# Kernel optimization log

Measured on AMD Instinct MI355X. Metric: run time of the kernel, lower is better.

Reference implementation:

```python
import jax, jax.numpy as jnp
import numpy as np

B, HH, WW, C, HEADS = 8, 56, 56, 384, 6
DIM_OUT = 384


def _upsample2x_bilinear(x):
    # x: [..., m, n] -> [..., 2m, 2n]; matches torch F.interpolate bilinear align_corners=False
    m, n = x.shape[-2], x.shape[-1]
    def coords(inn):
        c = (jnp.arange(2 * inn) + 0.5) / 2.0 - 0.5
        c = jnp.clip(c, 0.0, inn - 1)
        i0 = jnp.floor(c).astype(jnp.int32)
        i1 = jnp.minimum(i0 + 1, inn - 1)
        return i0, i1, (c - i0).astype(x.dtype)
    i0, i1, wy = coords(m)
    j0, j1, wx = coords(n)
    rows = x[..., i0, :] * (1 - wy)[:, None] + x[..., i1, :] * wy[:, None]
    return rows[..., :, j0] * (1 - wx) + rows[..., :, j1] * wx


def setup_inputs() -> dict:
    key = jax.random.key(0)
    ks = jax.random.split(key, 12)
    inp = {
        'x': jax.random.normal(ks[0], (B, HH * WW, C), jnp.float32),
        'res_attn': jax.random.normal(ks[1], (B, HEADS, (HH // 4) * (WW // 4), (HH // 2) * (WW // 2)), jnp.float32),
        'conv_q_w': jax.random.normal(ks[2], (C, 1, 3, 3), jnp.float32) * 0.05,
        'ln_g': jnp.ones((C,), jnp.float32),
        'ln_b': jnp.zeros((C,), jnp.float32),
        'wq': jax.random.normal(ks[3], (DIM_OUT, C), jnp.float32) * 0.02,
        'wk': jax.random.normal(ks[4], (DIM_OUT, C), jnp.float32) * 0.02,
        'wv': jax.random.normal(ks[5], (DIM_OUT, C), jnp.float32) * 0.02,
        'w_proj': jax.random.normal(ks[6], (DIM_OUT, DIM_OUT), jnp.float32) * 0.02,
        'b_proj': jnp.zeros((DIM_OUT,), jnp.float32),
        'w_fuse': jax.random.normal(ks[7], (HEADS, 2 * HEADS, 1, 1), jnp.float32) * 0.1,
        'b_fuse': jnp.zeros((HEADS,), jnp.float32),
        'h': HH,
        'w': WW,
    }
    return inp


def reference(x, res_attn, conv_q_w, ln_g, ln_b, wq, wk, wv, w_proj, b_proj, w_fuse, b_fuse, h, w):
    Bz, _, Cc = x.shape
    heads = w_fuse.shape[0]
    xi = x.transpose(0, 2, 1).reshape(Bz, Cc, h, w)  # b c h w
    # conv_proj_q: depthwise conv k3 s2 p1 (no bias), then LayerNorm
    q = jax.lax.conv_general_dilated(
        xi, conv_q_w, (2, 2), ((1, 1), (1, 1)),
        dimension_numbers=('NCHW', 'OIHW', 'NCHW'), feature_group_count=Cc)
    hq, wq2 = q.shape[2], q.shape[3]
    q = q.reshape(Bz, Cc, hq * wq2).transpose(0, 2, 1)  # b t c
    mu = q.mean(-1, keepdims=True)
    var = ((q - mu) ** 2).mean(-1, keepdims=True)
    q = (q - mu) / jnp.sqrt(var + 1e-5) * ln_g + ln_b
    # conv_proj_k/v: avg pool k2 s2 p0
    kv = xi.reshape(Bz, Cc, h // 2, 2, w // 2, 2).mean(axis=(3, 5))
    kv = kv.reshape(Bz, Cc, (h // 2) * (w // 2)).transpose(0, 2, 1)  # b t c
    dim_out = wq.shape[0]
    dh = dim_out // heads
    def split(t):
        return t.reshape(Bz, t.shape[1], heads, dh).transpose(0, 2, 1, 3)
    qh = split(q @ wq.T)
    kh = split(kv @ wk.T)
    vh = split(kv @ wv.T)
    scale = dim_out ** -0.5
    attn_score = jnp.einsum('bhlk,bhtk->bhlt', qh, kh) * scale  # [B,H,L,T]
    sh, sw = h // 4, w // 4
    a = res_attn.shape[-1]
    rx = res_attn[:, :, :sh * sw, :]
    rx = rx.reshape(Bz * heads, sh * sw, a).transpose(0, 2, 1).reshape(Bz * heads, a, sh, sw)
    rx = _upsample2x_bilinear(rx)  # (b h) a 2sh 2sw
    rx = rx.reshape(Bz, heads, a, 4 * sh * sw).transpose(0, 1, 3, 2)  # b h L a
    cat = jnp.concatenate([attn_score, rx], axis=1)  # [B, 2H, L, T]
    attn_score = jnp.einsum('bclt,oc->bolt', cat, w_fuse[:, :, 0, 0]) + b_fuse[None, :, None, None]
    attn = jax.nn.softmax(attn_score, axis=-1)
    out = jnp.einsum('bhlt,bhtv->bhlv', attn, vh)
    out = out.transpose(0, 2, 1, 3).reshape(Bz, -1, dim_out)
    return out @ w_proj.T + b_proj
```

## Files before the change

### kernel.cpp

```cpp
#include <hip/hip_runtime.h>

typedef unsigned int uint;
typedef unsigned short ushort_t;
typedef short bf16x8 __attribute__((ext_vector_type(8)));
typedef float f32x4 __attribute__((ext_vector_type(4)));

__device__ __forceinline__ ushort_t f2bf(float f) {
  uint u = __builtin_bit_cast(uint, f);
  u += 0x7fffu + ((u >> 16) & 1u);
  return (ushort_t)(u >> 16);
}
__device__ __forceinline__ float bf2f(ushort_t s) {
  return __builtin_bit_cast(float, (uint)s << 16);
}
__device__ __forceinline__ float bflo(uint u) { return __builtin_bit_cast(float, u << 16); }
__device__ __forceinline__ float bfhi(uint u) { return __builtin_bit_cast(float, u & 0xffff0000u); }
__device__ __forceinline__ bf16x8 ld_frag(const ushort_t* p) {
  return __builtin_bit_cast(bf16x8, *(const uint4*)p);
}

__global__ __launch_bounds__(384) void k_convln(
    const float* __restrict__ x, const float* __restrict__ wc,
    const float* __restrict__ g, const float* __restrict__ bb,
    ushort_t* __restrict__ qout)
{
  const int b  = blockIdx.x / 784;
  const int t  = blockIdx.x % 784;
  const int oy = t / 28, ox = t % 28;
  const int c  = threadIdx.x;
  const float* xb = x + (size_t)b * 3136 * 384 + c;
  float acc = 0.f;
  #pragma unroll
  for (int ky = 0; ky < 3; ky++) {
    const int iy = 2 * oy - 1 + ky;
    if (iy < 0 || iy >= 56) continue;
    #pragma unroll
    for (int kx = 0; kx < 3; kx++) {
      const int ix = 2 * ox - 1 + kx;
      if (ix < 0 || ix >= 56) continue;
      acc += wc[c * 9 + ky * 3 + kx] * xb[(size_t)(iy * 56 + ix) * 384];
    }
  }
  float s = acc, s2 = acc * acc;
  #pragma unroll
  for (int off = 32; off >= 1; off >>= 1) {
    s  += __shfl_xor(s,  off);
    s2 += __shfl_xor(s2, off);
  }
  __shared__ float ps[6], ps2[6];
  if ((c & 63) == 0) { ps[c >> 6] = s; ps2[c >> 6] = s2; }
  __syncthreads();
  float S = 0.f, S2 = 0.f;
  #pragma unroll
  for (int i = 0; i < 6; i++) { S += ps[i]; S2 += ps2[i]; }
  const float mu  = S * (1.f / 384.f);
  const float var = S2 * (1.f / 384.f) - mu * mu;
  const float inv = rsqrtf(var + 1e-5f);
  qout[((size_t)b * 784 + t) * 384 + c] = f2bf((acc - mu) * inv * g[c] + bb[c]);
}

__global__ __launch_bounds__(256) void k_pool(
    const float* __restrict__ x, ushort_t* __restrict__ kvout)
{
  const int idx = blockIdx.x * 256 + threadIdx.x;
  const int c = idx % 384;
  const int t = (idx / 384) % 784;
  const int b = idx / (384 * 784);
  const int ty = t / 28, tx = t % 28;
  const float* xb = x + (size_t)b * 3136 * 384 + c;
  const int r0 = (2 * ty) * 56 + 2 * tx;
  const float v = xb[(size_t)r0 * 384] + xb[(size_t)(r0 + 1) * 384]
                + xb[(size_t)(r0 + 56) * 384] + xb[(size_t)(r0 + 57) * 384];
  kvout[idx] = f2bf(v * 0.25f);
}

__global__ __launch_bounds__(256) void k_wcvt(
    const float* __restrict__ a, const float* __restrict__ b,
    const float* __restrict__ c, const float* __restrict__ d,
    ushort_t* __restrict__ oa, ushort_t* __restrict__ ob,
    ushort_t* __restrict__ oc, ushort_t* __restrict__ od)
{
  const int i = blockIdx.x * 256 + threadIdx.x;
  if (i < 147456) {
    oa[i] = f2bf(a[i]); ob[i] = f2bf(b[i]);
    oc[i] = f2bf(c[i]); od[i] = f2bf(d[i]);
  }
}

template<int MODE>
__global__ __launch_bounds__(256) void k_gemm(
    const ushort_t* __restrict__ X, const ushort_t* __restrict__ W,
    const float* __restrict__ bias, void* __restrict__ Y)
{
  __shared__ ushort_t As[128][40];
  __shared__ ushort_t Bs[128][40];
  const int tid = threadIdx.x, w = tid >> 6, lane = tid & 63;
  const int quad = lane >> 4, r = lane & 15;
  const int m0 = blockIdx.y * 128, n0 = blockIdx.x * 128;
  const int wm = w >> 1, wn = w & 1;
  const int lr = tid >> 2, lc = (tid & 3) << 3;
  const ushort_t* xp = X + (size_t)(m0 + lr) * 384 + lc;
  const ushort_t* wp = W + (size_t)(n0 + lr) * 384 + lc;
  f32x4 acc[4][4] = {};
  for (int k0 = 0; k0 < 384; k0 += 32) {
    __syncthreads();
    *(uint4*)&As[lr][lc]      = *(const uint4*)(xp + k0);
    *(uint4*)&As[lr + 64][lc] = *(const uint4*)(xp + (size_t)64 * 384 + k0);
    *(uint4*)&Bs[lr][lc]      = *(const uint4*)(wp + k0);
    *(uint4*)&Bs[lr + 64][lc] = *(const uint4*)(wp + (size_t)64 * 384 + k0);
    __syncthreads();
    bf16x8 af[4], bf_[4];
    #pragma unroll
    for (int mt = 0; mt < 4; mt++) af[mt]  = *(const bf16x8*)&As[wm * 64 + mt * 16 + r][quad * 8];
    #pragma unroll
    for (int nt = 0; nt < 4; nt++) bf_[nt] = *(const bf16x8*)&Bs[wn * 64 + nt * 16 + r][quad * 8];
    #pragma unroll
    for (int mt = 0; mt < 4; mt++)
      #pragma unroll
      for (int nt = 0; nt < 4; nt++)
        acc[mt][nt] = __builtin_amdgcn_mfma_f32_16x16x32_bf16(af[mt], bf_[nt], acc[mt][nt], 0, 0, 0);
  }
  #pragma unroll
  for (int mt = 0; mt < 4; mt++) {
    #pragma unroll
    for (int nt = 0; nt < 4; nt++) {
      #pragma unroll
      for (int i = 0; i < 4; i++) {
        const int row = m0 + wm * 64 + mt * 16 + quad * 4 + i;
        const int col = n0 + wn * 64 + nt * 16 + r;
        const float v = acc[mt][nt][i];
        if constexpr (MODE == 2) {
          ((float*)Y)[(size_t)row * 384 + col] = v + bias[col];
        } else if constexpr (MODE == 0) {
          ((ushort_t*)Y)[(size_t)row * 384 + col] = f2bf(v);
        } else {
          const int bb = row / 784, tt = row % 784;
          ((ushort_t*)Y)[((size_t)bb * 384 + col) * 784 + tt] = f2bf(v);
        }
      }
    }
  }
}

__global__ __launch_bounds__(256) void k_resmix(
    const float* __restrict__ ra, const float* __restrict__ w_fuse,
    const float* __restrict__ b_fuse, ushort_t* __restrict__ R)
{
  const int tid = threadIdx.x;
  const int b = blockIdx.x / 784, L = blockIdx.x % 784;
  __shared__ float w2[36], bfu[6];
  if (tid < 36) w2[tid] = w_fuse[(tid / 6) * 12 + 6 + (tid % 6)];
  if (tid < 6)  bfu[tid] = b_fuse[tid];
  __syncthreads();

  const int Yc = L / 28, Xc = L % 28;
  const float cy = fminf(fmaxf((float)Yc * 0.5f - 0.25f, 0.f), 13.f);
  const float cx = fminf(fmaxf((float)Xc * 0.5f - 0.25f, 0.f), 13.f);
  const int y0 = (int)cy, y1 = min(y0 + 1, 13);
  const int x0 = (int)cx, x1 = min(x0 + 1, 13);
  const float fy = cy - (float)y0, fx = cx - (float)x0;
  const float w00 = (1.f - fy) * (1.f - fx), w01 = (1.f - fy) * fx;
  const float w10 = fy * (1.f - fx),         w11 = fy * fx;
  const int p00 = (y0 * 14 + x0) * 784, p01 = (y0 * 14 + x1) * 784;
  const int p10 = (y1 * 14 + x0) * 784, p11 = (y1 * 14 + x1) * 784;

  const float* rab = ra + (size_t)b * 6 * 153664;
  ushort_t* Rrow = R + ((size_t)(b * 784 + L) * 6) * 784;

  for (int t = tid; t < 784; t += 256) {
    float U[6];
    #pragma unroll
    for (int c = 0; c < 6; c++) {
      const float* rc = rab + (size_t)c * 153664;
      U[c] = w00 * rc[p00 + t] + w01 * rc[p01 + t]
           + w10 * rc[p10 + t] + w11 * rc[p11 + t];
    }
    #pragma unroll
    for (int o = 0; o < 6; o++) {
      float v = bfu[o];
      #pragma unroll
      for (int c = 0; c < 6; c++) v += w2[o * 6 + c] * U[c];
      Rrow[(size_t)o * 784 + t] = f2bf(v);
    }
  }
}

__global__ __launch_bounds__(256, 3) void k_fattn(
    const ushort_t* __restrict__ Qb, const ushort_t* __restrict__ Kb,
    const ushort_t* __restrict__ Vt, const ushort_t* __restrict__ R,
    const float* __restrict__ w_fuse,
    float* __restrict__ Op, float* __restrict__ Ms, float* __restrict__ Ss)
{
  __shared__ ushort_t Ssc[6][16][72];
  __shared__ ushort_t Pl[6][16][72];
  __shared__ float m_st[6][16], s_st[6][16], a_st[6][16];
  __shared__ float w1[36];

  const int tid  = threadIdx.x;
  const int w    = tid >> 6, lane = tid & 63;
  const int quad = lane >> 4, r = lane & 15;
  const int b    = blockIdx.x & 7;
  const int m0   = (blockIdx.x >> 3) * 16;
  const int s    = blockIdx.y;
  const int tile0 = (s == 0) ? 0 : (3 * s + 1);
  const int tileN = (s == 0) ? 4 : 3;
  const float scale = 0.05103103630798288f;

  if (tid < 36) w1[tid] = w_fuse[(tid / 6) * 12 + (tid % 6)] * scale;
  if (tid < 96) { (&m_st[0][0])[tid] = -1e30f; (&s_st[0][0])[tid] = 0.f; }

  const ushort_t* qrow = Qb + ((size_t)(b * 784 + m0 + r)) * 384 + quad * 8;
  bf16x8 qf[6][2];
  #pragma unroll
  for (int h = 0; h < 6; h++) {
    qf[h][0] = ld_frag(qrow + h * 64);
    qf[h][1] = ld_frag(qrow + h * 64 + 32);
  }

  const int bl_l = tid >> 4, tq = tid & 15;
  const ushort_t* Rrow = R + ((size_t)(b * 784 + m0 + bl_l) * 6) * 784;

  const size_t kbase  = (size_t)b * 784 * 384;
  const size_t vtbase = (size_t)b * 384 * 784;

  f32x4 oacc[6] = {};

  for (int ii = 0; ii < tileN; ii++) {
    const int t0 = (tile0 + ii) * 64;

    {
      const int tA = min(t0 + w * 16 + r, 783);
      const ushort_t* krow = Kb + kbase + (size_t)tA * 384 + quad * 8;
      #pragma unroll
      for (int h = 0; h < 6; h++) {
        f32x4 sc = {};
        sc = __builtin_amdgcn_mfma_f32_16x16x32_bf16(qf[h][0], ld_frag(krow + h * 64),      sc, 0, 0, 0);
        sc = __builtin_amdgcn_mfma_f32_16x16x32_bf16(qf[h][1], ld_frag(krow + h * 64 + 32), sc, 0, 0, 0);
        #pragma unroll
        for (int i = 0; i < 4; i++)
          Ssc[h][quad * 4 + i][w * 16 + r] = f2bf(sc[i]);
      }
    }
    __syncthreads();

    {
      const int t4 = t0 + tq * 4;
      float F[6][4];
      #pragma unroll
      for (int o = 0; o < 6; o++) {
        const uint2 rv = *(const uint2*)(Rrow + (size_t)o * 784 + t4);
        F[o][0] = bflo(rv.x); F[o][1] = bfhi(rv.x);
        F[o][2] = bflo(rv.y); F[o][3] = bfhi(rv.y);
      }
      #pragma unroll
      for (int c = 0; c < 6; c++) {
        const uint2 sv = *(const uint2*)&Ssc[c][bl_l][tq * 4];
        const float s0 = bflo(sv.x), s1 = bfhi(sv.x);
        const float s2 = bflo(sv.y), s3 = bfhi(sv.y);
        #pragma unroll
        for (int o = 0; o < 6; o++) {
          const float wv = w1[o * 6 + c];
          F[o][0] += wv * s0; F[o][1] += wv * s1;
          F[o][2] += wv * s2; F[o][3] += wv * s3;
        }
      }
      #pragma unroll
      for (int j = 0; j < 4; j++) {
        if (t4 + j >= 784) {
          #pragma unroll
          for (int o = 0; o < 6; o++) F[o][j] = -1e30f;
        }
      }
      #pragma unroll
      for (int o = 0; o < 6; o++) {
        float mx = fmaxf(fmaxf(F[o][0], F[o][1]), fmaxf(F[o][2], F[o][3]));
        #pragma unroll
        for (int off = 8; off >= 1; off >>= 1) mx = fmaxf(mx, __shfl_xor(mx, off));
        const float m_old = m_st[o][bl_l];
        const float nm = fmaxf(m_old, mx);
        const float al = __expf(m_old - nm);
        float p0 = __expf(F[o][0] - nm), p1 = __expf(F[o][1] - nm);
        float p2 = __expf(F[o][2] - nm), p3 = __expf(F[o][3] - nm);
        float sm = p0 + p1 + p2 + p3;
        #pragma unroll
        for (int off = 8; off >= 1; off >>= 1) sm += __shfl_xor(sm, off);
        const uint lo = (uint)f2bf(p0) | ((uint)f2bf(p1) << 16);
        const uint hi = (uint)f2bf(p2) | ((uint)f2bf(p3) << 16);
        *(uint2*)&Pl[o][bl_l][tq * 4] = uint2{lo, hi};
        if (tq == 0) {
          m_st[o][bl_l] = nm;
          s_st[o][bl_l] = s_st[o][bl_l] * al + sm;
          a_st[o][bl_l] = al;
        }
      }
    }
    __syncthreads();

    #pragma unroll
    for (int o = 0; o < 6; o++) {
      const f32x4 al4 = *(const f32x4*)&a_st[o][quad * 4];
      oacc[o] *= al4;
      const bf16x8 pa0 = *(const bf16x8*)&Pl[o][r][quad * 8];
      const bf16x8 pa1 = *(const bf16x8*)&Pl[o][r][quad * 8 + 32];
      const ushort_t* vrow = Vt + vtbase + (size_t)(o * 64 + w * 16 + r) * 784 + t0 + quad * 8;
      oacc[o] = __builtin_amdgcn_mfma_f32_16x16x32_bf16(pa0, ld_frag(vrow),      oacc[o], 0, 0, 0);
      oacc[o] = __builtin_amdgcn_mfma_f32_16x16x32_bf16(pa1, ld_frag(vrow + 32), oacc[o], 0, 0, 0);
    }
    __syncthreads();
  }

  const size_t prow = (size_t)s * 6272 + (size_t)b * 784 + m0;
  #pragma unroll
  for (int o = 0; o < 6; o++) {
    #pragma unroll
    for (int i = 0; i < 4; i++) {
      Op[(prow + quad * 4 + i) * 384 + o * 64 + w * 16 + r] = oacc[o][i];
    }
  }
  if (tid < 96) {
    const int o = tid >> 4, l = tid & 15;
    Ms[(prow + l) * 6 + o] = m_st[o][l];
    Ss[(prow + l) * 6 + o] = s_st[o][l];
  }
}

__global__ __launch_bounds__(256) void k_comb(
    const float* __restrict__ Op, const float* __restrict__ Ms,
    const float* __restrict__ Ss, ushort_t* __restrict__ O)
{
  const int idx = blockIdx.x * 256 + threadIdx.x;
  const int row = idx / 384, col = idx % 384, o = col >> 6;
  float m = -1e30f;
  #pragma unroll
  for (int s = 0; s < 4; s++) m = fmaxf(m, Ms[((size_t)s * 6272 + row) * 6 + o]);
  float S = 0.f, acc = 0.f;
  #pragma unroll
  for (int s = 0; s < 4; s++) {
    const size_t pr = (size_t)s * 6272 + row;
    const float e = __expf(Ms[pr * 6 + o] - m);
    S   += Ss[pr * 6 + o] * e;
    acc += Op[pr * 384 + col] * e;
  }
  O[(size_t)row * 384 + col] = f2bf(acc / S);
}

extern "C" void kernel_launch(void* const* d_in, const int* in_sizes, int n_in,
                              void* d_out, int out_size, void* d_ws, size_t ws_size,
                              hipStream_t stream)
{
  const float* x        = (const float*)d_in[0];
  const float* res_attn = (const float*)d_in[1];
  const float* conv_w   = (const float*)d_in[2];
  const float* ln_g     = (const float*)d_in[3];
  const float* ln_b     = (const float*)d_in[4];
  const float* wq       = (const float*)d_in[5];
  const float* wk       = (const float*)d_in[6];
  const float* wv       = (const float*)d_in[7];
  const float* w_proj   = (const float*)d_in[8];
  const float* b_proj   = (const float*)d_in[9];
  const float* w_fuse   = (const float*)d_in[10];
  const float* b_fuse   = (const float*)d_in[11];
  float* out = (float*)d_out;

  const size_t NE = (size_t)8 * 784 * 384;
  const size_t NW = 147456;
  const size_t NR = (size_t)8 * 784 * 6 * 784;
  ushort_t* q_ln_b = (ushort_t*)d_ws;
  ushort_t* kv_b   = q_ln_b + NE;
  ushort_t* Qb     = kv_b + NE;
  ushort_t* Kb     = Qb + NE;
  ushort_t* Vt     = Kb + NE;
  ushort_t* Opre   = Vt + NE + 64;
  ushort_t* wqb    = Opre + NE;
  ushort_t* wkb    = wqb + NW;
  ushort_t* wvb    = wkb + NW;
  ushort_t* wpb    = wvb + NW;
  ushort_t* R      = wpb + NW;
  float*    Op     = (float*)(R + NR + 512);
  float*    Ms     = Op + 4 * NE;
  float*    Ss     = Ms + 4 * 6272 * 6;

  k_convln<<<dim3(8 * 784), dim3(384), 0, stream>>>(x, conv_w, ln_g, ln_b, q_ln_b);
  k_pool  <<<dim3(9408),    dim3(256), 0, stream>>>(x, kv_b);
  k_wcvt  <<<dim3(576),     dim3(256), 0, stream>>>(wq, wk, wv, w_proj, wqb, wkb, wvb, wpb);
  k_resmix<<<dim3(8 * 784), dim3(256), 0, stream>>>(res_attn, w_fuse, b_fuse, R);

  k_gemm<0><<<dim3(3, 49), dim3(256), 0, stream>>>(q_ln_b, wqb, nullptr, Qb);
  k_gemm<0><<<dim3(3, 49), dim3(256), 0, stream>>>(kv_b,   wkb, nullptr, Kb);
  k_gemm<1><<<dim3(3, 49), dim3(256), 0, stream>>>(kv_b,   wvb, nullptr, Vt);

  k_fattn<<<dim3(392, 4), dim3(256), 0, stream>>>(Qb, Kb, Vt, R, w_fuse, Op, Ms, Ss);
  k_comb <<<dim3(9408),   dim3(256), 0, stream>>>(Op, Ms, Ss, Opre);

  k_gemm<2><<<dim3(3, 49), dim3(256), 0, stream>>>(Opre, wpb, b_proj, out);
}
```

Baseline: 373.4 us.

## Apply residual-attention channel mix before upsampling and upsample inside the attention kernel

The 6x6 head-fusion mix on res_attn now runs at the low 14x14 resolution, writing a bf16 buffer a quarter the size of the old full upsampled R tensor. The attention kernel then does the bilinear 2x upsample on the fly with four gathered loads per element, which removes most of the R write and read traffic. Other changes: conv+LN and 2x2 pooling are merged into one kernel that reuses the conv taps, the V projection is a separate transposed GEMM whose stores are coalesced along tokens, attention partial outputs go through shared memory for float4 stores, and M/S statistics are packed as float2. The tradeoff is more scattered global loads and extra ALU work in the attention inner loop.

```diff
diff --git a/kernel.cpp b/kernel.cpp
--- a/kernel.cpp
+++ b/kernel.cpp
@@ -19,28 +19,32 @@
   return __builtin_bit_cast(bf16x8, *(const uint4*)p);
 }
 
-__global__ __launch_bounds__(384) void k_convln(
+__global__ __launch_bounds__(384) void k_prep(
     const float* __restrict__ x, const float* __restrict__ wc,
     const float* __restrict__ g, const float* __restrict__ bb,
-    ushort_t* __restrict__ qout)
+    ushort_t* __restrict__ qout, ushort_t* __restrict__ kvout)
 {
   const int b  = blockIdx.x / 784;
   const int t  = blockIdx.x % 784;
   const int oy = t / 28, ox = t % 28;
   const int c  = threadIdx.x;
   const float* xb = x + (size_t)b * 3136 * 384 + c;
-  float acc = 0.f;
+  float tap[9];
   #pragma unroll
   for (int ky = 0; ky < 3; ky++) {
     const int iy = 2 * oy - 1 + ky;
-    if (iy < 0 || iy >= 56) continue;
     #pragma unroll
     for (int kx = 0; kx < 3; kx++) {
       const int ix = 2 * ox - 1 + kx;
-      if (ix < 0 || ix >= 56) continue;
-      acc += wc[c * 9 + ky * 3 + kx] * xb[(size_t)(iy * 56 + ix) * 384];
-    }
-  }
+      tap[ky * 3 + kx] = (iy >= 0 && iy < 56 && ix >= 0 && ix < 56)
+                         ? xb[(size_t)(iy * 56 + ix) * 384] : 0.f;
+    }
+  }
+  float acc = 0.f;
+  #pragma unroll
+  for (int k = 0; k < 9; k++) acc += wc[c * 9 + k] * tap[k];
+  const float pool = (tap[4] + tap[5] + tap[7] + tap[8]) * 0.25f;
+
   float s = acc, s2 = acc * acc;
   #pragma unroll
   for (int off = 32; off >= 1; off >>= 1) {
@@ -56,22 +60,9 @@
   const float mu  = S * (1.f / 384.f);
   const float var = S2 * (1.f / 384.f) - mu * mu;
   const float inv = rsqrtf(var + 1e-5f);
-  qout[((size_t)b * 784 + t) * 384 + c] = f2bf((acc - mu) * inv * g[c] + bb[c]);
-}
-
-__global__ __launch_bounds__(256) void k_pool(
-    const float* __restrict__ x, ushort_t* __restrict__ kvout)
-{
-  const int idx = blockIdx.x * 256 + threadIdx.x;
-  const int c = idx % 384;
-  const int t = (idx / 384) % 784;
-  const int b = idx / (384 * 784);
-  const int ty = t / 28, tx = t % 28;
-  const float* xb = x + (size_t)b * 3136 * 384 + c;
-  const int r0 = (2 * ty) * 56 + 2 * tx;
-  const float v = xb[(size_t)r0 * 384] + xb[(size_t)(r0 + 1) * 384]
-                + xb[(size_t)(r0 + 56) * 384] + xb[(size_t)(r0 + 57) * 384];
-  kvout[idx] = f2bf(v * 0.25f);
+  const size_t o = ((size_t)b * 784 + t) * 384 + c;
+  qout[o]  = f2bf((acc - mu) * inv * g[c] + bb[c]);
+  kvout[o] = f2bf(pool);
 }
 
 __global__ __launch_bounds__(256) void k_wcvt(
@@ -84,6 +75,31 @@
   if (i < 147456) {
     oa[i] = f2bf(a[i]); ob[i] = f2bf(b[i]);
     oc[i] = f2bf(c[i]); od[i] = f2bf(d[i]);
+  }
+}
+
+__global__ __launch_bounds__(256) void k_rcmix(
+    const float* __restrict__ ra, const float* __restrict__ w_fuse,
+    ushort_t* __restrict__ RC)
+{
+  const int tid = threadIdx.x;
+  const int b = blockIdx.x / 196, lc = blockIdx.x % 196;
+  __shared__ float w2[36];
+  if (tid < 36) w2[tid] = w_fuse[(tid / 6) * 12 + 6 + (tid % 6)];
+  __syncthreads();
+  const float* rab = ra + ((size_t)b * 6 * 196 + lc) * 784;
+  ushort_t* RCb = RC + ((size_t)b * 6 * 196 + lc) * 784;
+  for (int t = tid; t < 784; t += 256) {
+    float U[6];
+    #pragma unroll
+    for (int c = 0; c < 6; c++) U[c] = rab[(size_t)c * 153664 + t];
+    #pragma unroll
+    for (int o = 0; o < 6; o++) {
+      float v = 0.f;
+      #pragma unroll
+      for (int c = 0; c < 6; c++) v += w2[o * 6 + c] * U[c];
+      RCb[(size_t)o * 153664 + t] = f2bf(v);
+    }
   }
 }
 
@@ -129,72 +145,74 @@
         const int row = m0 + wm * 64 + mt * 16 + quad * 4 + i;
         const int col = n0 + wn * 64 + nt * 16 + r;
         const float v = acc[mt][nt][i];
-        if constexpr (MODE == 2) {
-          ((float*)Y)[(size_t)row * 384 + col] = v + bias[col];
-        } else if constexpr (MODE == 0) {
-          ((ushort_t*)Y)[(size_t)row * 384 + col] = f2bf(v);
-        } else {
-          const int bb = row / 784, tt = row % 784;
-          ((ushort_t*)Y)[((size_t)bb * 384 + col) * 784 + tt] = f2bf(v);
-        }
-      }
-    }
-  }
-}
-
-__global__ __launch_bounds__(256) void k_resmix(
-    const float* __restrict__ ra, const float* __restrict__ w_fuse,
-    const float* __restrict__ b_fuse, ushort_t* __restrict__ R)
-{
-  const int tid = threadIdx.x;
-  const int b = blockIdx.x / 784, L = blockIdx.x % 784;
-  __shared__ float w2[36], bfu[6];
-  if (tid < 36) w2[tid] = w_fuse[(tid / 6) * 12 + 6 + (tid % 6)];
-  if (tid < 6)  bfu[tid] = b_fuse[tid];
-  __syncthreads();
-
-  const int Yc = L / 28, Xc = L % 28;
-  const float cy = fminf(fmaxf((float)Yc * 0.5f - 0.25f, 0.f), 13.f);
-  const float cx = fminf(fmaxf((float)Xc * 0.5f - 0.25f, 0.f), 13.f);
-  const int y0 = (int)cy, y1 = min(y0 + 1, 13);
-  const int x0 = (int)cx, x1 = min(x0 + 1, 13);
-  const float fy = cy - (float)y0, fx = cx - (float)x0;
-  const float w00 = (1.f - fy) * (1.f - fx), w01 = (1.f - fy) * fx;
-  const float w10 = fy * (1.f - fx),         w11 = fy * fx;
-  const int p00 = (y0 * 14 + x0) * 784, p01 = (y0 * 14 + x1) * 784;
-  const int p10 = (y1 * 14 + x0) * 784, p11 = (y1 * 14 + x1) * 784;
-
-  const float* rab = ra + (size_t)b * 6 * 153664;
-  ushort_t* Rrow = R + ((size_t)(b * 784 + L) * 6) * 784;
-
-  for (int t = tid; t < 784; t += 256) {
-    float U[6];
-    #pragma unroll
-    for (int c = 0; c < 6; c++) {
-      const float* rc = rab + (size_t)c * 153664;
-      U[c] = w00 * rc[p00 + t] + w01 * rc[p01 + t]
-           + w10 * rc[p10 + t] + w11 * rc[p11 + t];
-    }
-    #pragma unroll
-    for (int o = 0; o < 6; o++) {
-      float v = bfu[o];
-      #pragma unroll
-      for (int c = 0; c < 6; c++) v += w2[o * 6 + c] * U[c];
-      Rrow[(size_t)o * 784 + t] = f2bf(v);
+        if constexpr (MODE == 2) ((float*)Y)[(size_t)row * 384 + col] = v + bias[col];
+        else                     ((ushort_t*)Y)[(size_t)row * 384 + col] = f2bf(v);
+      }
+    }
+  }
+}
+
+__global__ __launch_bounds__(256) void k_gemmT(
+    const ushort_t* __restrict__ W, const ushort_t* __restrict__ X,
+    ushort_t* __restrict__ Vt)
+{
+  __shared__ ushort_t As[128][40];
+  __shared__ ushort_t Bs[128][40];
+  const int tid = threadIdx.x, w = tid >> 6, lane = tid & 63;
+  const int quad = lane >> 4, r = lane & 15;
+  const int m0 = blockIdx.y * 128, n0 = blockIdx.x * 128;
+  const int wm = w >> 1, wn = w & 1;
+  const int lr = tid >> 2, lc = (tid & 3) << 3;
+  const ushort_t* ap = W + (size_t)(m0 + lr) * 384 + lc;
+  const ushort_t* bp = X + (size_t)(n0 + lr) * 384 + lc;
+  f32x4 acc[4][4] = {};
+  for (int k0 = 0; k0 < 384; k0 += 32) {
+    __syncthreads();
+    *(uint4*)&As[lr][lc]      = *(const uint4*)(ap + k0);
+    *(uint4*)&As[lr + 64][lc] = *(const uint4*)(ap + (size_t)64 * 384 + k0);
+    *(uint4*)&Bs[lr][lc]      = *(const uint4*)(bp + k0);
+    *(uint4*)&Bs[lr + 64][lc] = *(const uint4*)(bp + (size_t)64 * 384 + k0);
+    __syncthreads();
+    bf16x8 af[4], bf_[4];
+    #pragma unroll
+    for (int mt = 0; mt < 4; mt++) af[mt]  = *(const bf16x8*)&As[wm * 64 + mt * 16 + r][quad * 8];
+    #pragma unroll
+    for (int nt = 0; nt < 4; nt++) bf_[nt] = *(const bf16x8*)&Bs[wn * 64 + nt * 16 + r][quad * 8];
+    #pragma unroll
+    for (int mt = 0; mt < 4; mt++)
+      #pragma unroll
+      for (int nt = 0; nt < 4; nt++)
+        acc[mt][nt] = __builtin_amdgcn_mfma_f32_16x16x32_bf16(af[mt], bf_[nt], acc[mt][nt], 0, 0, 0);
+  }
+  #pragma unroll
+  for (int mt = 0; mt < 4; mt++) {
+    #pragma unroll
+    for (int nt = 0; nt < 4; nt++) {
+      #pragma unroll
+      for (int i = 0; i < 4; i++) {
+        const int d   = m0 + wm * 64 + mt * 16 + quad * 4 + i;
+        const int tok = n0 + wn * 64 + nt * 16 + r;
+        const int b = tok / 784, tt = tok % 784;
+        Vt[((size_t)b * 384 + d) * 784 + tt] = f2bf(acc[mt][nt][i]);
+      }
     }
   }
 }
 
 __global__ __launch_bounds__(256, 3) void k_fattn(
     const ushort_t* __restrict__ Qb, const ushort_t* __restrict__ Kb,
-    const ushort_t* __restrict__ Vt, const ushort_t* __restrict__ R,
-    const float* __restrict__ w_fuse,
-    float* __restrict__ Op, float* __restrict__ Ms, float* __restrict__ Ss)
-{
-  __shared__ ushort_t Ssc[6][16][72];
-  __shared__ ushort_t Pl[6][16][72];
+    const ushort_t* __restrict__ Vt, const ushort_t* __restrict__ RC,
+    const float* __restrict__ w_fuse, const float* __restrict__ b_fuse,
+    float* __restrict__ Op, float2* __restrict__ MS)
+{
+  __shared__ char smem[27648];
+  ushort_t* Ssc_ = (ushort_t*)smem;
+  ushort_t* Pl_  = (ushort_t*)(smem + 13824);
+  float*    stage = (float*)smem;
+  #define SSC(h, l, t) Ssc_[(((h) * 16 + (l)) * 72) + (t)]
+  #define PL(h, l, t)  Pl_[(((h) * 16 + (l)) * 72) + (t)]
   __shared__ float m_st[6][16], s_st[6][16], a_st[6][16];
-  __shared__ float w1[36];
+  __shared__ float w1[36], bfu[6];
 
   const int tid  = threadIdx.x;
   const int w    = tid >> 6, lane = tid & 63;
@@ -207,6 +225,7 @@
   const float scale = 0.05103103630798288f;
 
   if (tid < 36) w1[tid] = w_fuse[(tid / 6) * 12 + (tid % 6)] * scale;
+  if (tid < 6)  bfu[tid] = b_fuse[tid];
   if (tid < 96) { (&m_st[0][0])[tid] = -1e30f; (&s_st[0][0])[tid] = 0.f; }
 
   const ushort_t* qrow = Qb + ((size_t)(b * 784 + m0 + r)) * 384 + quad * 8;
@@ -218,7 +237,18 @@
   }
 
   const int bl_l = tid >> 4, tq = tid & 15;
-  const ushort_t* Rrow = R + ((size_t)(b * 784 + m0 + bl_l) * 6) * 784;
+  const int L = m0 + bl_l;
+  const int Yc = L / 28, Xc = L % 28;
+  const float cy = fminf(fmaxf((float)Yc * 0.5f - 0.25f, 0.f), 13.f);
+  const float cx = fminf(fmaxf((float)Xc * 0.5f - 0.25f, 0.f), 13.f);
+  const int y0 = (int)cy, y1 = min(y0 + 1, 13);
+  const int x0 = (int)cx, x1 = min(x0 + 1, 13);
+  const float fy = cy - (float)y0, fx = cx - (float)x0;
+  const float w00 = (1.f - fy) * (1.f - fx), w01 = (1.f - fy) * fx;
+  const float w10 = fy * (1.f - fx),         w11 = fy * fx;
+  const int q00 = (y0 * 14 + x0) * 784, q01 = (y0 * 14 + x1) * 784;
+  const int q10 = (y1 * 14 + x0) * 784, q11 = (y1 * 14 + x1) * 784;
+  const ushort_t* RCb = RC + (size_t)b * 6 * 153664;
 
   const size_t kbase  = (size_t)b * 784 * 384;
   const size_t vtbase = (size_t)b * 384 * 784;
@@ -238,7 +268,7 @@
         sc = __builtin_amdgcn_mfma_f32_16x16x32_bf16(qf[h][1], ld_frag(krow + h * 64 + 32), sc, 0, 0, 0);
         #pragma unroll
         for (int i = 0; i < 4; i++)
-          Ssc[h][quad * 4 + i][w * 16 + r] = f2bf(sc[i]);
+          SSC(h, quad * 4 + i, w * 16 + r) = f2bf(sc[i]);
       }
     }
     __syncthreads();
@@ -248,13 +278,19 @@
       float F[6][4];
       #pragma unroll
       for (int o = 0; o < 6; o++) {
-        const uint2 rv = *(const uint2*)(Rrow + (size_t)o * 784 + t4);
-        F[o][0] = bflo(rv.x); F[o][1] = bfhi(rv.x);
-        F[o][2] = bflo(rv.y); F[o][3] = bfhi(rv.y);
+        const ushort_t* rco = RCb + (size_t)o * 153664 + t4;
+        const uint2 u00 = *(const uint2*)(rco + q00);
+        const uint2 u01 = *(const uint2*)(rco + q01);
+        const uint2 u10 = *(const uint2*)(rco + q10);
+        const uint2 u11 = *(const uint2*)(rco + q11);
+        F[o][0] = bfu[o] + w00 * bflo(u00.x) + w01 * bflo(u01.x) + w10 * bflo(u10.x) + w11 * bflo(u11.x);
+        F[o][1] = bfu[o] + w00 * bfhi(u00.x) + w01 * bfhi(u01.x) + w10 * bfhi(u10.x) + w11 * bfhi(u11.x);
+        F[o][2] = bfu[o] + w00 * bflo(u00.y) + w01 * bflo(u01.y) + w10 * bflo(u10.y) + w11 * bflo(u11.y);
+        F[o][3] = bfu[o] + w00 * bfhi(u00.y) + w01 * bfhi(u01.y) + w10 * bfhi(u10.y) + w11 * bfhi(u11.y);
       }
       #pragma unroll
       for (int c = 0; c < 6; c++) {
-        const uint2 sv = *(const uint2*)&Ssc[c][bl_l][tq * 4];
+        const uint2 sv = *(const uint2*)&SSC(c, bl_l, tq * 4);
         const float s0 = bflo(sv.x), s1 = bfhi(sv.x);
         const float s2 = bflo(sv.y), s3 = bfhi(sv.y);
         #pragma unroll
@@ -286,7 +322,7 @@
         for (int off = 8; off >= 1; off >>= 1) sm += __shfl_xor(sm, off);
         const uint lo = (uint)f2bf(p0) | ((uint)f2bf(p1) << 16);
         const uint hi = (uint)f2bf(p2) | ((uint)f2bf(p3) << 16);
-        *(uint2*)&Pl[o][bl_l][tq * 4] = uint2{lo, hi};
+        *(uint2*)&PL(o, bl_l, tq * 4) = uint2{lo, hi};
         if (tq == 0) {
           m_st[o][bl_l] = nm;
           s_st[o][bl_l] = s_st[o][bl_l] * al + sm;
@@ -300,8 +336,8 @@
     for (int o = 0; o < 6; o++) {
       const f32x4 al4 = *(const f32x4*)&a_st[o][quad * 4];
       oacc[o] *= al4;
-      const bf16x8 pa0 = *(const bf16x8*)&Pl[o][r][quad * 8];
-      const bf16x8 pa1 = *(const bf16x8*)&Pl[o][r][quad * 8 + 32];
+      const bf16x8 pa0 = *(const bf16x8*)&PL(o, r, quad * 8);
+      const bf16x8 pa1 = *(const bf16x8*)&PL(o, r, quad * 8 + 32);
       const ushort_t* vrow = Vt + vtbase + (size_t)(o * 64 + w * 16 + r) * 784 + t0 + quad * 8;
       oacc[o] = __builtin_amdgcn_mfma_f32_16x16x32_bf16(pa0, ld_frag(vrow),      oacc[o], 0, 0, 0);
       oacc[o] = __builtin_amdgcn_mfma_f32_16x16x32_bf16(pa1, ld_frag(vrow + 32), oacc[o], 0, 0, 0);
@@ -309,37 +345,43 @@
     __syncthreads();
   }
 
+  #pragma unroll
+  for (int o = 0; o < 6; o++)
+    #pragma unroll
+    for (int i = 0; i < 4; i++)
+      stage[(quad * 4 + i) * 392 + o * 64 + w * 16 + r] = oacc[o][i];
+  __syncthreads();
   const size_t prow = (size_t)s * 6272 + (size_t)b * 784 + m0;
   #pragma unroll
-  for (int o = 0; o < 6; o++) {
-    #pragma unroll
-    for (int i = 0; i < 4; i++) {
-      Op[(prow + quad * 4 + i) * 384 + o * 64 + w * 16 + r] = oacc[o][i];
-    }
+  for (int j = 0; j < 6; j++) {
+    const int idx = tid + j * 256;
+    const int row = idx / 96, c4 = idx % 96;
+    *(float4*)&Op[(prow + row) * 384 + c4 * 4] = *(const float4*)&stage[row * 392 + c4 * 4];
   }
   if (tid < 96) {
-    const int o = tid >> 4, l = tid & 15;
-    Ms[(prow + l) * 6 + o] = m_st[o][l];
-    Ss[(prow + l) * 6 + o] = s_st[o][l];
-  }
+    const int l = tid / 6, o = tid % 6;
+    MS[(prow + l) * 6 + o] = float2{m_st[o][l], s_st[o][l]};
+  }
+  #undef SSC
+  #undef PL
 }
 
 __global__ __launch_bounds__(256) void k_comb(
-    const float* __restrict__ Op, const float* __restrict__ Ms,
-    const float* __restrict__ Ss, ushort_t* __restrict__ O)
+    const float* __restrict__ Op, const float2* __restrict__ MS,
+    ushort_t* __restrict__ O)
 {
   const int idx = blockIdx.x * 256 + threadIdx.x;
   const int row = idx / 384, col = idx % 384, o = col >> 6;
-  float m = -1e30f;
-  #pragma unroll
-  for (int s = 0; s < 4; s++) m = fmaxf(m, Ms[((size_t)s * 6272 + row) * 6 + o]);
+  float2 ms[4];
+  #pragma unroll
+  for (int s = 0; s < 4; s++) ms[s] = MS[((size_t)s * 6272 + row) * 6 + o];
+  float m = fmaxf(fmaxf(ms[0].x, ms[1].x), fmaxf(ms[2].x, ms[3].x));
   float S = 0.f, acc = 0.f;
   #pragma unroll
   for (int s = 0; s < 4; s++) {
-    const size_t pr = (size_t)s * 6272 + row;
-    const float e = __expf(Ms[pr * 6 + o] - m);
-    S   += Ss[pr * 6 + o] * e;
-    acc += Op[pr * 384 + col] * e;
+    const float e = __expf(ms[s].x - m);
+    S   += ms[s].y * e;
+    acc += Op[((size_t)s * 6272 + row) * 384 + col] * e;
   }
   O[(size_t)row * 384 + col] = f2bf(acc / S);
 }
@@ -362,9 +404,9 @@
   const float* b_fuse   = (const float*)d_in[11];
   float* out = (float*)d_out;
 
-  const size_t NE = (size_t)8 * 784 * 384;
-  const size_t NW = 147456;
-  const size_t NR = (size_t)8 * 784 * 6 * 784;
+  const size_t NE  = (size_t)8 * 784 * 384;
+  const size_t NW  = 147456;
+  const size_t NRC = (size_t)8 * 6 * 196 * 784;
   ushort_t* q_ln_b = (ushort_t*)d_ws;
   ushort_t* kv_b   = q_ln_b + NE;
   ushort_t* Qb     = kv_b + NE;
@@ -375,22 +417,20 @@
   ushort_t* wkb    = wqb + NW;
   ushort_t* wvb    = wkb + NW;
   ushort_t* wpb    = wvb + NW;
-  ushort_t* R      = wpb + NW;
-  float*    Op     = (float*)(R + NR + 512);
-  float*    Ms     = Op + 4 * NE;
-  float*    Ss     = Ms + 4 * 6272 * 6;
-
-  k_convln<<<dim3(8 * 784), dim3(384), 0, stream>>>(x, conv_w, ln_g, ln_b, q_ln_b);
-  k_pool  <<<dim3(9408),    dim3(256), 0, stream>>>(x, kv_b);
-  k_wcvt  <<<dim3(576),     dim3(256), 0, stream>>>(wq, wk, wv, w_proj, wqb, wkb, wvb, wpb);
-  k_resmix<<<dim3(8 * 784), dim3(256), 0, stream>>>(res_attn, w_fuse, b_fuse, R);
+  ushort_t* RC     = wpb + NW;
+  float*    Op     = (float*)(RC + NRC + 64);
+  float2*   MS     = (float2*)(Op + 4 * NE);
+
+  k_prep <<<dim3(8 * 784), dim3(384), 0, stream>>>(x, conv_w, ln_g, ln_b, q_ln_b, kv_b);
+  k_wcvt <<<dim3(576),     dim3(256), 0, stream>>>(wq, wk, wv, w_proj, wqb, wkb, wvb, wpb);
+  k_rcmix<<<dim3(8 * 196), dim3(256), 0, stream>>>(res_attn, w_fuse, RC);
 
   k_gemm<0><<<dim3(3, 49), dim3(256), 0, stream>>>(q_ln_b, wqb, nullptr, Qb);
   k_gemm<0><<<dim3(3, 49), dim3(256), 0, stream>>>(kv_b,   wkb, nullptr, Kb);
-  k_gemm<1><<<dim3(3, 49), dim3(256), 0, stream>>>(kv_b,   wvb, nullptr, Vt);
-
-  k_fattn<<<dim3(392, 4), dim3(256), 0, stream>>>(Qb, Kb, Vt, R, w_fuse, Op, Ms, Ss);
-  k_comb <<<dim3(9408),   dim3(256), 0, stream>>>(Op, Ms, Ss, Opre);
+  k_gemmT  <<<dim3(49, 3), dim3(256), 0, stream>>>(wvb, kv_b, Vt);
+
+  k_fattn<<<dim3(392, 4), dim3(256), 0, stream>>>(Qb, Kb, Vt, RC, w_fuse, b_fuse, Op, MS);
+  k_comb <<<dim3(9408),   dim3(256), 0, stream>>>(Op, MS, Opre);
 
   k_gemm<2><<<dim3(3, 49), dim3(256), 0, stream>>>(Opre, wpb, b_proj, out);
 }
```

Result: faster. 354.2 us (-5.2%).
